# Optimization experiments

Measured on AMD Instinct MI355X. Metric: run time of the kernel, lower is better.

Reference implementation:

```python
import jax, jax.numpy as jnp
import numpy as np

N_NODES = 50000
N_EDGES = 800000
NODE_DIM = 128
EMBED_DIM = 128


def _gcn_conv(x, W, b, src, dst):
    """GCNConv: y = D^{-1/2} (A + I) D^{-1/2} X W + b (unit edge weights)."""
    n = x.shape[0]
    xw = x @ W  # [N, out]
    loop = jnp.arange(n, dtype=src.dtype)
    src2 = jnp.concatenate([src, loop])  # self-loops appended
    dst2 = jnp.concatenate([dst, loop])
    w2 = jnp.ones(src2.shape[0], dtype=xw.dtype)
    deg = jax.ops.segment_sum(w2, dst2, num_segments=n)
    dinv = jnp.where(deg > 0, jax.lax.rsqrt(deg), jnp.zeros_like(deg))
    norm = dinv[src2] * w2 * dinv[dst2]  # [E+N]
    out = jax.ops.segment_sum(norm[:, None] * xw[src2], dst2, num_segments=n)
    return out + b


def setup_inputs() -> dict:
    key = jax.random.key(0)
    ks = jax.random.split(key, 20)
    inp = {
        'node_feat': jax.random.normal(ks[0], (N_NODES, NODE_DIM), dtype=jnp.float32),
        'src': jax.random.randint(ks[1], (N_EDGES,), 0, N_NODES, dtype=jnp.int64) if jax.config.jax_enable_x64 else jax.random.randint(ks[1], (N_EDGES,), 0, N_NODES),
        'dst': jax.random.randint(ks[2], (N_EDGES,), 0, N_NODES),
        'h': jax.random.normal(ks[3], (N_NODES, EMBED_DIM), dtype=jnp.float32),
    }
    sc_in = 1.0 / np.sqrt(NODE_DIM)
    sc_2e = 1.0 / np.sqrt(2 * EMBED_DIM)
    sc_e = 1.0 / np.sqrt(EMBED_DIM)
    # conv weight/bias + gate linear weight/bias for z, r, h gates
    for i, g in enumerate(['z', 'r', 'hh']):
        inp[f'Wc_{g}'] = jax.random.normal(ks[4 + 4 * i], (NODE_DIM, EMBED_DIM), dtype=jnp.float32) * sc_in
        inp[f'bc_{g}'] = jnp.zeros((EMBED_DIM,), dtype=jnp.float32)
        inp[f'Wl_{g}'] = jax.random.normal(ks[5 + 4 * i], (2 * EMBED_DIM, EMBED_DIM), dtype=jnp.float32) * sc_2e
        inp[f'bl_{g}'] = jnp.zeros((EMBED_DIM,), dtype=jnp.float32)
    inp['W_lin'] = jax.random.normal(ks[16], (EMBED_DIM, EMBED_DIM), dtype=jnp.float32) * sc_e
    inp['b_lin'] = jnp.zeros((EMBED_DIM,), dtype=jnp.float32)
    return inp


def reference(node_feat, src, dst, h,
              Wc_z, bc_z, Wl_z, bl_z,
              Wc_r, bc_r, Wl_r, bl_r,
              Wc_hh, bc_hh, Wl_hh, bl_hh,
              W_lin, b_lin):
    # TGCN GRU cell
    cz = _gcn_conv(node_feat, Wc_z, bc_z, src, dst)
    Z = jax.nn.sigmoid(jnp.concatenate([cz, h], axis=1) @ Wl_z + bl_z)
    cr = _gcn_conv(node_feat, Wc_r, bc_r, src, dst)
    R = jax.nn.sigmoid(jnp.concatenate([cr, h], axis=1) @ Wl_r + bl_r)
    ch = _gcn_conv(node_feat, Wc_hh, bc_hh, src, dst)
    H_tilde = jnp.tanh(jnp.concatenate([ch, h * R], axis=1) @ Wl_hh + bl_hh)
    h_0 = Z * h + (1.0 - Z) * H_tilde
    # wrapper: relu + linear
    z_out = jax.nn.relu(h_0) @ W_lin + b_lin
    return (z_out, h_0)
```

## Files before the change

### kernel.cpp

```cpp
#include <hip/hip_runtime.h>
#include <math.h>

#define NN 50000
#define DD 128
#define EE 800000

typedef __attribute__((ext_vector_type(8))) short short8;
typedef __attribute__((ext_vector_type(4))) float f32x4;

__device__ __forceinline__ ushort f2bf(float f) {
    union { float f; unsigned u; } v; v.f = f;
    unsigned r = v.u + 0x7FFF + ((v.u >> 16) & 1);
    return (ushort)(r >> 16);
}

__global__ void k_cvt_deg(const float* __restrict__ X, ushort* __restrict__ Xb,
                          const int* __restrict__ dste, int* __restrict__ deg) {
    int i = blockIdx.x * 256 + threadIdx.x;
    float4 v = ((const float4*)X)[i];
    ushort4 u;
    u.x = f2bf(v.x); u.y = f2bf(v.y); u.z = f2bf(v.z); u.w = f2bf(v.w);
    ((ushort4*)Xb)[i] = u;
    if (i < EE) atomicAdd(&deg[dste[i]], 1);
}

__global__ void k_alloc(const int* __restrict__ deg, int* __restrict__ off,
                        int* __restrict__ cursor, float* __restrict__ dinv) {
    int n = blockIdx.x * 256 + threadIdx.x;
    int lane = threadIdx.x & 63;
    int d = (n < NN) ? deg[n] : 0;
    int x = d;
    #pragma unroll
    for (int o = 1; o < 64; o <<= 1) {
        int y = __shfl_up(x, o);
        if (lane >= o) x += y;
    }
    int total = __shfl(x, 63);
    int base = 0;
    if (lane == 0) base = atomicAdd(cursor, total);
    base = __shfl(base, 0);
    if (n < NN) {
        off[n] = base + x - d;
        dinv[n] = rsqrtf((float)d + 1.0f);
    }
}

__global__ void k_fill(const int* __restrict__ src, const int* __restrict__ dst,
                       const int* __restrict__ off, int* __restrict__ cur,
                       int* __restrict__ csr) {
    int e = blockIdx.x * 256 + threadIdx.x;
    if (e < EE) {
        int d = dst[e];
        int slot = atomicAdd(&cur[d], 1);
        csr[off[d] + slot] = src[e];
    }
}

__global__ __launch_bounds__(256) void k_gather(const ushort* __restrict__ Xb,
                                                const int* __restrict__ csr,
                                                const int* __restrict__ off,
                                                const int* __restrict__ deg,
                                                const float* __restrict__ dinv,
                                                ushort* __restrict__ AXb) {
    int tid = blockIdx.x * 256 + threadIdx.x;
    int n = tid >> 6, lane = tid & 63;
    if (n >= NN) return;
    float dd = dinv[n];
    uint a = *((const uint*)(Xb + (size_t)n * 128 + lane * 2));
    float acc0 = dd * dd * __uint_as_float(a << 16);
    float acc1 = dd * dd * __uint_as_float(a & 0xffff0000u);
    int o = off[n], cnt = deg[n];
    int i = 0;
    for (; i + 8 <= cnt; i += 8) {
        int s[8];
        #pragma unroll
        for (int u = 0; u < 8; u++) s[u] = csr[o + i + u];
        uint v[8];
        #pragma unroll
        for (int u = 0; u < 8; u++) v[u] = *((const uint*)(Xb + (size_t)s[u] * 128 + lane * 2));
        float c[8];
        #pragma unroll
        for (int u = 0; u < 8; u++) c[u] = dinv[s[u]] * dd;
        #pragma unroll
        for (int u = 0; u < 8; u++) {
            acc0 += c[u] * __uint_as_float(v[u] << 16);
            acc1 += c[u] * __uint_as_float(v[u] & 0xffff0000u);
        }
    }
    for (; i < cnt; i++) {
        int s = csr[o + i];
        float c = dinv[s] * dd;
        uint v = *((const uint*)(Xb + (size_t)s * 128 + lane * 2));
        acc0 += c * __uint_as_float(v << 16);
        acc1 += c * __uint_as_float(v & 0xffff0000u);
    }
    ushort2 u2; u2.x = f2bf(acc0); u2.y = f2bf(acc1);
    *((ushort2*)(AXb + (size_t)n * 128 + lane * 2)) = u2;
}

__global__ void k_prep(const float* __restrict__ Wc_z, const float* __restrict__ Wl_z,
                       const float* __restrict__ bc_z, const float* __restrict__ bl_z,
                       const float* __restrict__ Wc_r, const float* __restrict__ Wl_r,
                       const float* __restrict__ bc_r, const float* __restrict__ bl_r,
                       const float* __restrict__ Wc_h, const float* __restrict__ Wl_h,
                       const float* __restrict__ bc_h, const float* __restrict__ bl_h,
                       const float* __restrict__ W_lin,
                       ushort* __restrict__ WAs, ushort* __restrict__ WBs,
                       ushort* __restrict__ WLs, float* __restrict__ bA,
                       float* __restrict__ bB) {
    int idx = blockIdx.x * 256 + threadIdx.x;
    if (idx < 65536) {
        int k = idx >> 8, c = idx & 255, cc = c & 127;
        const float* Wc = (c < 128) ? Wc_z : Wc_r;
        const float* Wl = (c < 128) ? Wl_z : Wl_r;
        float v;
        if (k < 128) {
            float s = 0.f;
            for (int j = 0; j < 128; j++) s += Wc[k * 128 + j] * Wl[j * 128 + cc];
            v = s;
        } else {
            v = Wl[k * 128 + cc];
        }
        WAs[(k >> 5) * 8192 + (c >> 4) * 512 + (((k >> 3) & 3) * 16 + (c & 15)) * 8 + (k & 7)] = f2bf(v);
    } else if (idx < 98304) {
        int i2 = idx - 65536;
        int k = i2 >> 7, c = i2 & 127;
        float v;
        if (k < 128) {
            float s = 0.f;
            for (int j = 0; j < 128; j++) s += Wc_h[k * 128 + j] * Wl_h[j * 128 + c];
            v = s;
        } else {
            v = Wl_h[k * 128 + c];
        }
        WBs[(k >> 5) * 4096 + (c >> 4) * 512 + (((k >> 3) & 3) * 16 + (c & 15)) * 8 + (k & 7)] = f2bf(v);
    } else if (idx < 114688) {
        int i3 = idx - 98304;
        int k = i3 >> 7, c = i3 & 127;
        WLs[(k >> 5) * 4096 + (c >> 4) * 512 + (((k >> 3) & 3) * 16 + (c & 15)) * 8 + (k & 7)] = f2bf(W_lin[k * 128 + c]);
    } else if (idx < 114944) {
        int c = idx - 114688, cc = c & 127;
        const float* bc = (c < 128) ? bc_z : bc_r;
        const float* Wl = (c < 128) ? Wl_z : Wl_r;
        const float* bl = (c < 128) ? bl_z : bl_r;
        float s = bl[cc];
        for (int j = 0; j < 128; j++) s += bc[j] * Wl[j * 128 + cc];
        bA[c] = s;
    } else if (idx < 115072) {
        int c = idx - 114944;
        float s = bl_h[c];
        for (int j = 0; j < 128; j++) s += bc_h[j] * Wl_h[j * 128 + c];
        bB[c] = s;
    }
}

__global__ __launch_bounds__(256) void k_fused(const ushort* __restrict__ AXb,
                                               const float* __restrict__ h,
                                               const ushort* __restrict__ WAs,
                                               const ushort* __restrict__ WBs,
                                               const ushort* __restrict__ WLs,
                                               const float* __restrict__ bA,
                                               const float* __restrict__ bB,
                                               const float* __restrict__ b_lin,
                                               float* __restrict__ out_z,
                                               float* __restrict__ out_h) {
    __shared__ uint4 WbufV[2][1024];
    __shared__ __align__(16) ushort hRbuf[8192];

    const int tid = threadIdx.x;
    const int row0 = blockIdx.x * 64;
    const int lane = tid & 63, w = tid >> 6;
    const int tx = lane & 15, g = lane >> 4;
    const int arow = w * 16 + tx;
    const int gar = row0 + arow;
    const int drow = w * 16 + g * 4;
    const int aswz = (arow & 7) << 4;

    short8 z8 = {0, 0, 0, 0, 0, 0, 0, 0};
    short8 axf[4], hf[4];
    bool av = (gar < NN);
    #pragma unroll
    for (int ks = 0; ks < 4; ks++)
        axf[ks] = av ? *((const short8*)(AXb + (size_t)gar * 128 + ks * 32 + g * 8)) : z8;
    {
        const float4* hp = (const float4*)(h + (size_t)gar * 128);
        #pragma unroll
        for (int ks = 0; ks < 4; ks++) {
            if (av) {
                float4 u0 = hp[ks * 8 + g * 2];
                float4 u1 = hp[ks * 8 + g * 2 + 1];
                short8 t;
                t[0] = (short)f2bf(u0.x); t[1] = (short)f2bf(u0.y);
                t[2] = (short)f2bf(u0.z); t[3] = (short)f2bf(u0.w);
                t[4] = (short)f2bf(u1.x); t[5] = (short)f2bf(u1.y);
                t[6] = (short)f2bf(u1.z); t[7] = (short)f2bf(u1.w);
                hf[ks] = t;
            } else hf[ks] = z8;
        }
    }

    uint4 sr[4];
    const uint4* gwA = (const uint4*)WAs;

    #pragma unroll
    for (int j = 0; j < 4; j++) sr[j] = gwA[j * 256 + tid];
    #pragma unroll
    for (int j = 0; j < 4; j++) WbufV[0][j * 256 + tid] = sr[j];
    #pragma unroll
    for (int j = 0; j < 4; j++) sr[j] = gwA[1024 + j * 256 + tid];
    __syncthreads();

    f32x4 accA[16];
    #pragma unroll
    for (int ct = 0; ct < 16; ct++) accA[ct] = (f32x4){0.f, 0.f, 0.f, 0.f};

    #pragma unroll
    for (int ks = 0; ks < 8; ks++) {
        const int cur = ks & 1, nxt = cur ^ 1;
        if (ks < 7) {
            #pragma unroll
            for (int j = 0; j < 4; j++) WbufV[nxt][j * 256 + tid] = sr[j];
        }
        if (ks < 6) {
            #pragma unroll
            for (int j = 0; j < 4; j++) sr[j] = gwA[(ks + 2) * 1024 + j * 256 + tid];
        }
        const ushort* wbp = (const ushort*)WbufV[cur];
        short8 a = (ks < 4) ? axf[ks] : hf[ks - 4];
        #pragma unroll
        for (int ct = 0; ct < 16; ct++) {
            short8 b = *((const short8*)(wbp + ct * 512 + lane * 8));
            accA[ct] = __builtin_amdgcn_mfma_f32_16x16x32_bf16(a, b, accA[ct], 0, 0, 0);
        }
        __syncthreads();
    }

    float Zv[8][4], hv[8][4];
    #pragma unroll
    for (int ct = 0; ct < 8; ct++) {
        float bias = bA[ct * 16 + tx];
        #pragma unroll
        for (int r = 0; r < 4; r++)
            Zv[ct][r] = 1.f / (1.f + expf(-(accA[ct][r] + bias)));
    }
    #pragma unroll
    for (int ct = 0; ct < 8; ct++) {
        int cc = ct * 16 + tx;
        float bias = bA[128 + cc];
        #pragma unroll
        for (int r = 0; r < 4; r++) {
            int rr = drow + r, gr = row0 + rr;
            float hval = (gr < NN) ? h[(size_t)gr * 128 + cc] : 0.f;
            hv[ct][r] = hval;
            float R = 1.f / (1.f + expf(-(accA[8 + ct][r] + bias)));
            *((ushort*)((char*)hRbuf + rr * 256 + ((cc * 2) ^ ((rr & 7) << 4)))) = f2bf(hval * R);
        }
    }

    const uint4* gwB = (const uint4*)WBs;
    #pragma unroll
    for (int j = 0; j < 2; j++) sr[j] = gwB[j * 256 + tid];
    #pragma unroll
    for (int j = 0; j < 2; j++) WbufV[0][j * 256 + tid] = sr[j];
    #pragma unroll
    for (int j = 0; j < 2; j++) sr[j] = gwB[512 + j * 256 + tid];
    __syncthreads();

    f32x4 accB[8];
    #pragma unroll
    for (int ct = 0; ct < 8; ct++) accB[ct] = (f32x4){0.f, 0.f, 0.f, 0.f};

    #pragma unroll
    for (int ks = 0; ks < 8; ks++) {
        const int cur = ks & 1, nxt = cur ^ 1;
        if (ks < 7) {
            #pragma unroll
            for (int j = 0; j < 2; j++) WbufV[nxt][j * 256 + tid] = sr[j];
        }
        if (ks < 6) {
            #pragma unroll
            for (int j = 0; j < 2; j++) sr[j] = gwB[(ks + 2) * 512 + j * 256 + tid];
        }
        const ushort* wbp = (const ushort*)WbufV[cur];
        short8 a;
        if (ks < 4) {
            a = axf[ks];
        } else {
            int kk = ks - 4;
            a = *((const short8*)((const char*)hRbuf + arow * 256 + ((kk * 64 + g * 16) ^ aswz)));
        }
        #pragma unroll
        for (int ct = 0; ct < 8; ct++) {
            short8 b = *((const short8*)(wbp + ct * 512 + lane * 8));
            accB[ct] = __builtin_amdgcn_mfma_f32_16x16x32_bf16(a, b, accB[ct], 0, 0, 0);
        }
        __syncthreads();
    }

    #pragma unroll
    for (int ct = 0; ct < 8; ct++) {
        int cc = ct * 16 + tx;
        float bias = bB[cc];
        #pragma unroll
        for (int r = 0; r < 4; r++) {
            int rr = drow + r, gr = row0 + rr;
            float gv = accB[ct][r] + bias;
            float H = tanhf(gv);
            float Z = Zv[ct][r];
            float h0 = Z * hv[ct][r] + (1.f - Z) * H;
            if (gr < NN) out_h[(size_t)gr * 128 + cc] = h0;
            *((ushort*)((char*)hRbuf + rr * 256 + ((cc * 2) ^ ((rr & 7) << 4)))) = f2bf(fmaxf(h0, 0.f));
        }
    }

    const uint4* gwL = (const uint4*)WLs;
    #pragma unroll
    for (int j = 0; j < 2; j++) sr[j] = gwL[j * 256 + tid];
    #pragma unroll
    for (int j = 0; j < 2; j++) WbufV[0][j * 256 + tid] = sr[j];
    #pragma unroll
    for (int j = 0; j < 2; j++) sr[j] = gwL[512 + j * 256 + tid];
    __syncthreads();

    f32x4 accC[8];
    #pragma unroll
    for (int ct = 0; ct < 8; ct++) accC[ct] = (f32x4){0.f, 0.f, 0.f, 0.f};

    #pragma unroll
    for (int ks = 0; ks < 4; ks++) {
        const int cur = ks & 1, nxt = cur ^ 1;
        if (ks < 3) {
            #pragma unroll
            for (int j = 0; j < 2; j++) WbufV[nxt][j * 256 + tid] = sr[j];
        }
        if (ks < 2) {
            #pragma unroll
            for (int j = 0; j < 2; j++) sr[j] = gwL[(ks + 2) * 512 + j * 256 + tid];
        }
        const ushort* wbp = (const ushort*)WbufV[cur];
        short8 a = *((const short8*)((const char*)hRbuf + arow * 256 + ((ks * 64 + g * 16) ^ aswz)));
        #pragma unroll
        for (int ct = 0; ct < 8; ct++) {
            short8 b = *((const short8*)(wbp + ct * 512 + lane * 8));
            accC[ct] = __builtin_amdgcn_mfma_f32_16x16x32_bf16(a, b, accC[ct], 0, 0, 0);
        }
        __syncthreads();
    }

    #pragma unroll
    for (int ct = 0; ct < 8; ct++) {
        int cc = ct * 16 + tx;
        float bias = b_lin[cc];
        #pragma unroll
        for (int r = 0; r < 4; r++) {
            int gr = row0 + drow + r;
            if (gr < NN) out_z[(size_t)gr * 128 + cc] = accC[ct][r] + bias;
        }
    }
}


extern "C" void kernel_launch(void* const* d_in, const int* in_sizes, int n_in,
                              void* d_out, int out_size, void* d_ws, size_t ws_size,
                              hipStream_t stream) {
    const float* X    = (const float*)d_in[0];
    const int*   src  = (const int*)d_in[1];
    const int*   dst  = (const int*)d_in[2];
    const float* h    = (const float*)d_in[3];
    const float* Wc_z = (const float*)d_in[4];
    const float* bc_z = (const float*)d_in[5];
    const float* Wl_z = (const float*)d_in[6];
    const float* bl_z = (const float*)d_in[7];
    const float* Wc_r = (const float*)d_in[8];
    const float* bc_r = (const float*)d_in[9];
    const float* Wl_r = (const float*)d_in[10];
    const float* bl_r = (const float*)d_in[11];
    const float* Wc_h = (const float*)d_in[12];
    const float* bc_h = (const float*)d_in[13];
    const float* Wl_h = (const float*)d_in[14];
    const float* bl_h = (const float*)d_in[15];
    const float* W_lin = (const float*)d_in[16];
    const float* b_lin = (const float*)d_in[17];

    float* out_z = (float*)d_out;
    float* out_h = out_z + (size_t)NN * DD;

    float* ws = (float*)d_ws;
    float*  dinv   = ws;
    int*    deg    = (int*)(ws + 50048);
    int*    cur    = (int*)(ws + 100096);
    int*    cursor = (int*)(ws + 150144);
    int*    off    = (int*)(ws + 150208);
    int*    csr    = (int*)(ws + 200256);
    float*  bA     = ws + 1000320;
    float*  bB     = ws + 1000576;
    ushort* WAs    = (ushort*)(ws + 1000704);
    ushort* WBs    = (ushort*)(ws + 1033472);
    ushort* WLs    = (ushort*)(ws + 1049856);
    ushort* AXb    = (ushort*)(ws + 1058048);
    ushort* Xb     = (ushort*)(ws + 4258048);

    hipMemsetAsync(deg, 0, 100160 * sizeof(int), stream);
    k_prep<<<450, 256, 0, stream>>>(Wc_z, Wl_z, bc_z, bl_z, Wc_r, Wl_r, bc_r, bl_r,
                                    Wc_h, Wl_h, bc_h, bl_h, W_lin,
                                    WAs, WBs, WLs, bA, bB);
    k_cvt_deg<<<6250, 256, 0, stream>>>(X, Xb, dst, deg);
    k_alloc<<<196, 256, 0, stream>>>(deg, off, cursor, dinv);
    k_fill<<<3125, 256, 0, stream>>>(src, dst, off, cur, csr);
    k_gather<<<12500, 256, 0, stream>>>(Xb, csr, off, deg, dinv, AXb);
    k_fused<<<782, 256, 0, stream>>>(AXb, h, WAs, WBs, WLs, bA, bB, b_lin, out_z, out_h);
}
```

Baseline: 350.8 us.

## Split fused GRU GEMM into three persistent kernels with register-resident weights

Replaces the single fused per-64-row GEMM kernel with three persistent kernels (gates Z/R, candidate H, output linear). Each keeps its weight fragments in registers and grid-strides over 16-row subtiles, so weights are no longer streamed through LDS for every block. Also merges the X/h bf16 conversion with weight prep into one launch, and has the CSR fill use a precomputed cursor instead of off+slot. The cost is extra global traffic for the Zt, hR and relu intermediates and two more kernel launches.

```diff
diff --git a/kernel.cpp b/kernel.cpp
--- a/kernel.cpp
+++ b/kernel.cpp
@@ -4,6 +4,7 @@
 #define NN 50000
 #define DD 128
 #define EE 800000
+#define NSUB 3125
 
 typedef __attribute__((ext_vector_type(8))) short short8;
 typedef __attribute__((ext_vector_type(4))) float f32x4;
@@ -13,102 +14,42 @@
     unsigned r = v.u + 0x7FFF + ((v.u >> 16) & 1);
     return (ushort)(r >> 16);
 }
-
-__global__ void k_cvt_deg(const float* __restrict__ X, ushort* __restrict__ Xb,
-                          const int* __restrict__ dste, int* __restrict__ deg) {
-    int i = blockIdx.x * 256 + threadIdx.x;
-    float4 v = ((const float4*)X)[i];
-    ushort4 u;
-    u.x = f2bf(v.x); u.y = f2bf(v.y); u.z = f2bf(v.z); u.w = f2bf(v.w);
-    ((ushort4*)Xb)[i] = u;
-    if (i < EE) atomicAdd(&deg[dste[i]], 1);
-}
-
-__global__ void k_alloc(const int* __restrict__ deg, int* __restrict__ off,
-                        int* __restrict__ cursor, float* __restrict__ dinv) {
-    int n = blockIdx.x * 256 + threadIdx.x;
-    int lane = threadIdx.x & 63;
-    int d = (n < NN) ? deg[n] : 0;
-    int x = d;
-    #pragma unroll
-    for (int o = 1; o < 64; o <<= 1) {
-        int y = __shfl_up(x, o);
-        if (lane >= o) x += y;
-    }
-    int total = __shfl(x, 63);
-    int base = 0;
-    if (lane == 0) base = atomicAdd(cursor, total);
-    base = __shfl(base, 0);
-    if (n < NN) {
-        off[n] = base + x - d;
-        dinv[n] = rsqrtf((float)d + 1.0f);
-    }
-}
-
-__global__ void k_fill(const int* __restrict__ src, const int* __restrict__ dst,
-                       const int* __restrict__ off, int* __restrict__ cur,
-                       int* __restrict__ csr) {
-    int e = blockIdx.x * 256 + threadIdx.x;
-    if (e < EE) {
-        int d = dst[e];
-        int slot = atomicAdd(&cur[d], 1);
-        csr[off[d] + slot] = src[e];
-    }
-}
-
-__global__ __launch_bounds__(256) void k_gather(const ushort* __restrict__ Xb,
-                                                const int* __restrict__ csr,
-                                                const int* __restrict__ off,
-                                                const int* __restrict__ deg,
-                                                const float* __restrict__ dinv,
-                                                ushort* __restrict__ AXb) {
-    int tid = blockIdx.x * 256 + threadIdx.x;
-    int n = tid >> 6, lane = tid & 63;
-    if (n >= NN) return;
-    float dd = dinv[n];
-    uint a = *((const uint*)(Xb + (size_t)n * 128 + lane * 2));
-    float acc0 = dd * dd * __uint_as_float(a << 16);
-    float acc1 = dd * dd * __uint_as_float(a & 0xffff0000u);
-    int o = off[n], cnt = deg[n];
-    int i = 0;
-    for (; i + 8 <= cnt; i += 8) {
-        int s[8];
-        #pragma unroll
-        for (int u = 0; u < 8; u++) s[u] = csr[o + i + u];
-        uint v[8];
-        #pragma unroll
-        for (int u = 0; u < 8; u++) v[u] = *((const uint*)(Xb + (size_t)s[u] * 128 + lane * 2));
-        float c[8];
-        #pragma unroll
-        for (int u = 0; u < 8; u++) c[u] = dinv[s[u]] * dd;
-        #pragma unroll
-        for (int u = 0; u < 8; u++) {
-            acc0 += c[u] * __uint_as_float(v[u] << 16);
-            acc1 += c[u] * __uint_as_float(v[u] & 0xffff0000u);
-        }
-    }
-    for (; i < cnt; i++) {
-        int s = csr[o + i];
-        float c = dinv[s] * dd;
-        uint v = *((const uint*)(Xb + (size_t)s * 128 + lane * 2));
-        acc0 += c * __uint_as_float(v << 16);
-        acc1 += c * __uint_as_float(v & 0xffff0000u);
-    }
-    ushort2 u2; u2.x = f2bf(acc0); u2.y = f2bf(acc1);
-    *((ushort2*)(AXb + (size_t)n * 128 + lane * 2)) = u2;
-}
-
-__global__ void k_prep(const float* __restrict__ Wc_z, const float* __restrict__ Wl_z,
-                       const float* __restrict__ bc_z, const float* __restrict__ bl_z,
-                       const float* __restrict__ Wc_r, const float* __restrict__ Wl_r,
-                       const float* __restrict__ bc_r, const float* __restrict__ bl_r,
-                       const float* __restrict__ Wc_h, const float* __restrict__ Wl_h,
-                       const float* __restrict__ bc_h, const float* __restrict__ bl_h,
-                       const float* __restrict__ W_lin,
-                       ushort* __restrict__ WAs, ushort* __restrict__ WBs,
-                       ushort* __restrict__ WLs, float* __restrict__ bA,
-                       float* __restrict__ bB) {
-    int idx = blockIdx.x * 256 + threadIdx.x;
+__device__ __forceinline__ float bf2f(ushort u) {
+    return __uint_as_float(((unsigned)u) << 16);
+}
+__device__ __forceinline__ float sigm(float x) { return 1.f / (1.f + expf(-x)); }
+
+__global__ void k_cvtprep(const float* __restrict__ X, ushort* __restrict__ Xb,
+                          const float* __restrict__ h, ushort* __restrict__ hb,
+                          const int* __restrict__ dste, int* __restrict__ deg,
+                          const float* __restrict__ Wc_z, const float* __restrict__ Wl_z,
+                          const float* __restrict__ bc_z, const float* __restrict__ bl_z,
+                          const float* __restrict__ Wc_r, const float* __restrict__ Wl_r,
+                          const float* __restrict__ bc_r, const float* __restrict__ bl_r,
+                          const float* __restrict__ Wc_h, const float* __restrict__ Wl_h,
+                          const float* __restrict__ bc_h, const float* __restrict__ bl_h,
+                          const float* __restrict__ W_lin,
+                          ushort* __restrict__ WAs, ushort* __restrict__ WBs,
+                          ushort* __restrict__ WLs, float* __restrict__ bA,
+                          float* __restrict__ bB) {
+    if (blockIdx.x < 6250) {
+        int i = blockIdx.x * 256 + threadIdx.x;
+        float4 v = ((const float4*)X)[i];
+        ushort4 u;
+        u.x = f2bf(v.x); u.y = f2bf(v.y); u.z = f2bf(v.z); u.w = f2bf(v.w);
+        ((ushort4*)Xb)[i] = u;
+        if (i < EE) atomicAdd(&deg[dste[i]], 1);
+        return;
+    }
+    if (blockIdx.x < 12500) {
+        int i = (blockIdx.x - 6250) * 256 + threadIdx.x;
+        float4 v = ((const float4*)h)[i];
+        ushort4 u;
+        u.x = f2bf(v.x); u.y = f2bf(v.y); u.z = f2bf(v.z); u.w = f2bf(v.w);
+        ((ushort4*)hb)[i] = u;
+        return;
+    }
+    int idx = (blockIdx.x - 12500) * 256 + threadIdx.x;
     if (idx < 65536) {
         int k = idx >> 8, c = idx & 255, cc = c & 127;
         const float* Wc = (c < 128) ? Wc_z : Wc_r;
@@ -154,207 +95,270 @@
     }
 }
 
-__global__ __launch_bounds__(256) void k_fused(const ushort* __restrict__ AXb,
-                                               const float* __restrict__ h,
-                                               const ushort* __restrict__ WAs,
-                                               const ushort* __restrict__ WBs,
-                                               const ushort* __restrict__ WLs,
-                                               const float* __restrict__ bA,
-                                               const float* __restrict__ bB,
-                                               const float* __restrict__ b_lin,
-                                               float* __restrict__ out_z,
-                                               float* __restrict__ out_h) {
-    __shared__ uint4 WbufV[2][1024];
-    __shared__ __align__(16) ushort hRbuf[8192];
-
-    const int tid = threadIdx.x;
-    const int row0 = blockIdx.x * 64;
-    const int lane = tid & 63, w = tid >> 6;
+__global__ void k_alloc(const int* __restrict__ deg, int* __restrict__ off,
+                        int* __restrict__ cur, int* __restrict__ cursor,
+                        float* __restrict__ dinv) {
+    int n = blockIdx.x * 256 + threadIdx.x;
+    int lane = threadIdx.x & 63;
+    int d = (n < NN) ? deg[n] : 0;
+    int x = d;
+    #pragma unroll
+    for (int o = 1; o < 64; o <<= 1) {
+        int y = __shfl_up(x, o);
+        if (lane >= o) x += y;
+    }
+    int total = __shfl(x, 63);
+    int base = 0;
+    if (lane == 0) base = atomicAdd(cursor, total);
+    base = __shfl(base, 0);
+    if (n < NN) {
+        int o2 = base + x - d;
+        off[n] = o2;
+        cur[n] = o2;
+        dinv[n] = rsqrtf((float)d + 1.0f);
+    }
+}
+
+__global__ void k_fill(const int* __restrict__ src, const int* __restrict__ dst,
+                       int* __restrict__ cur, int* __restrict__ csr) {
+    int e = blockIdx.x * 256 + threadIdx.x;
+    if (e < EE) {
+        int slot = atomicAdd(&cur[dst[e]], 1);
+        csr[slot] = src[e];
+    }
+}
+
+__global__ __launch_bounds__(256) void k_gather(const ushort* __restrict__ Xb,
+                                                const int* __restrict__ csr,
+                                                const int* __restrict__ off,
+                                                const int* __restrict__ deg,
+                                                const float* __restrict__ dinv,
+                                                ushort* __restrict__ AXb) {
+    int tid = blockIdx.x * 256 + threadIdx.x;
+    int n = tid >> 6, lane = tid & 63;
+    if (n >= NN) return;
+    int o   = __builtin_amdgcn_readfirstlane(off[n]);
+    int cnt = __builtin_amdgcn_readfirstlane(deg[n]);
+    float dd = dinv[n];
+    uint a = *((const uint*)(Xb + (size_t)n * 128 + lane * 2));
+    float acc0 = dd * dd * __uint_as_float(a << 16);
+    float acc1 = dd * dd * __uint_as_float(a & 0xffff0000u);
+    int i = 0;
+    for (; i + 8 <= cnt; i += 8) {
+        int s[8];
+        #pragma unroll
+        for (int u = 0; u < 8; u++) s[u] = csr[o + i + u];
+        uint v[8];
+        #pragma unroll
+        for (int u = 0; u < 8; u++) v[u] = *((const uint*)(Xb + (size_t)s[u] * 128 + lane * 2));
+        float c[8];
+        #pragma unroll
+        for (int u = 0; u < 8; u++) c[u] = dinv[s[u]] * dd;
+        #pragma unroll
+        for (int u = 0; u < 8; u++) {
+            acc0 += c[u] * __uint_as_float(v[u] << 16);
+            acc1 += c[u] * __uint_as_float(v[u] & 0xffff0000u);
+        }
+    }
+    for (; i < cnt; i++) {
+        int s = csr[o + i];
+        float c = dinv[s] * dd;
+        uint v = *((const uint*)(Xb + (size_t)s * 128 + lane * 2));
+        acc0 += c * __uint_as_float(v << 16);
+        acc1 += c * __uint_as_float(v & 0xffff0000u);
+    }
+    ushort2 u2; u2.x = f2bf(acc0); u2.y = f2bf(acc1);
+    *((ushort2*)(AXb + (size_t)n * 128 + lane * 2)) = u2;
+}
+
+__global__ __launch_bounds__(256, 2) void k_gemmA(const ushort* __restrict__ AXb,
+                                                  const ushort* __restrict__ hb,
+                                                  const float* __restrict__ h,
+                                                  const ushort* __restrict__ WAs,
+                                                  const float* __restrict__ bA,
+                                                  ushort* __restrict__ Zt,
+                                                  ushort* __restrict__ hRb) {
+    __shared__ ushort scr[4][1024];
+    const int tid = threadIdx.x, lane = tid & 63, w = tid >> 6;
     const int tx = lane & 15, g = lane >> 4;
-    const int arow = w * 16 + tx;
-    const int gar = row0 + arow;
-    const int drow = w * 16 + g * 4;
-    const int aswz = (arow & 7) << 4;
-
-    short8 z8 = {0, 0, 0, 0, 0, 0, 0, 0};
-    short8 axf[4], hf[4];
-    bool av = (gar < NN);
-    #pragma unroll
-    for (int ks = 0; ks < 4; ks++)
-        axf[ks] = av ? *((const short8*)(AXb + (size_t)gar * 128 + ks * 32 + g * 8)) : z8;
-    {
-        const float4* hp = (const float4*)(h + (size_t)gar * 128);
+
+    short8 wf[4][8];
+    #pragma unroll
+    for (int ct = 0; ct < 4; ct++)
+        #pragma unroll
+        for (int ks = 0; ks < 8; ks++)
+            wf[ct][ks] = *((const short8*)(WAs + ks * 8192 + (w * 4 + ct) * 512 + lane * 8));
+    float bias[4];
+    #pragma unroll
+    for (int ct = 0; ct < 4; ct++) bias[ct] = bA[w * 64 + ct * 16 + tx];
+
+    for (int rs = blockIdx.x; rs < NSUB; rs += gridDim.x) {
+        const int arow = rs * 16 + tx;
+        short8 axf[4], hf[4];
         #pragma unroll
         for (int ks = 0; ks < 4; ks++) {
-            if (av) {
-                float4 u0 = hp[ks * 8 + g * 2];
-                float4 u1 = hp[ks * 8 + g * 2 + 1];
-                short8 t;
-                t[0] = (short)f2bf(u0.x); t[1] = (short)f2bf(u0.y);
-                t[2] = (short)f2bf(u0.z); t[3] = (short)f2bf(u0.w);
-                t[4] = (short)f2bf(u1.x); t[5] = (short)f2bf(u1.y);
-                t[6] = (short)f2bf(u1.z); t[7] = (short)f2bf(u1.w);
-                hf[ks] = t;
-            } else hf[ks] = z8;
-        }
-    }
-
-    uint4 sr[4];
-    const uint4* gwA = (const uint4*)WAs;
-
-    #pragma unroll
-    for (int j = 0; j < 4; j++) sr[j] = gwA[j * 256 + tid];
-    #pragma unroll
-    for (int j = 0; j < 4; j++) WbufV[0][j * 256 + tid] = sr[j];
-    #pragma unroll
-    for (int j = 0; j < 4; j++) sr[j] = gwA[1024 + j * 256 + tid];
-    __syncthreads();
-
-    f32x4 accA[16];
-    #pragma unroll
-    for (int ct = 0; ct < 16; ct++) accA[ct] = (f32x4){0.f, 0.f, 0.f, 0.f};
-
-    #pragma unroll
-    for (int ks = 0; ks < 8; ks++) {
-        const int cur = ks & 1, nxt = cur ^ 1;
-        if (ks < 7) {
-            #pragma unroll
-            for (int j = 0; j < 4; j++) WbufV[nxt][j * 256 + tid] = sr[j];
-        }
-        if (ks < 6) {
-            #pragma unroll
-            for (int j = 0; j < 4; j++) sr[j] = gwA[(ks + 2) * 1024 + j * 256 + tid];
-        }
-        const ushort* wbp = (const ushort*)WbufV[cur];
-        short8 a = (ks < 4) ? axf[ks] : hf[ks - 4];
-        #pragma unroll
-        for (int ct = 0; ct < 16; ct++) {
-            short8 b = *((const short8*)(wbp + ct * 512 + lane * 8));
-            accA[ct] = __builtin_amdgcn_mfma_f32_16x16x32_bf16(a, b, accA[ct], 0, 0, 0);
-        }
-        __syncthreads();
-    }
-
-    float Zv[8][4], hv[8][4];
-    #pragma unroll
-    for (int ct = 0; ct < 8; ct++) {
-        float bias = bA[ct * 16 + tx];
-        #pragma unroll
-        for (int r = 0; r < 4; r++)
-            Zv[ct][r] = 1.f / (1.f + expf(-(accA[ct][r] + bias)));
-    }
-    #pragma unroll
-    for (int ct = 0; ct < 8; ct++) {
-        int cc = ct * 16 + tx;
-        float bias = bA[128 + cc];
-        #pragma unroll
-        for (int r = 0; r < 4; r++) {
-            int rr = drow + r, gr = row0 + rr;
-            float hval = (gr < NN) ? h[(size_t)gr * 128 + cc] : 0.f;
-            hv[ct][r] = hval;
-            float R = 1.f / (1.f + expf(-(accA[8 + ct][r] + bias)));
-            *((ushort*)((char*)hRbuf + rr * 256 + ((cc * 2) ^ ((rr & 7) << 4)))) = f2bf(hval * R);
-        }
-    }
-
-    const uint4* gwB = (const uint4*)WBs;
-    #pragma unroll
-    for (int j = 0; j < 2; j++) sr[j] = gwB[j * 256 + tid];
-    #pragma unroll
-    for (int j = 0; j < 2; j++) WbufV[0][j * 256 + tid] = sr[j];
-    #pragma unroll
-    for (int j = 0; j < 2; j++) sr[j] = gwB[512 + j * 256 + tid];
-    __syncthreads();
-
-    f32x4 accB[8];
-    #pragma unroll
-    for (int ct = 0; ct < 8; ct++) accB[ct] = (f32x4){0.f, 0.f, 0.f, 0.f};
-
-    #pragma unroll
-    for (int ks = 0; ks < 8; ks++) {
-        const int cur = ks & 1, nxt = cur ^ 1;
-        if (ks < 7) {
-            #pragma unroll
-            for (int j = 0; j < 2; j++) WbufV[nxt][j * 256 + tid] = sr[j];
-        }
-        if (ks < 6) {
-            #pragma unroll
-            for (int j = 0; j < 2; j++) sr[j] = gwB[(ks + 2) * 512 + j * 256 + tid];
-        }
-        const ushort* wbp = (const ushort*)WbufV[cur];
-        short8 a;
-        if (ks < 4) {
-            a = axf[ks];
+            axf[ks] = *((const short8*)(AXb + (size_t)arow * 128 + ks * 32 + g * 8));
+            hf[ks]  = *((const short8*)(hb  + (size_t)arow * 128 + ks * 32 + g * 8));
+        }
+        f32x4 acc[4];
+        #pragma unroll
+        for (int ct = 0; ct < 4; ct++) acc[ct] = (f32x4){0.f, 0.f, 0.f, 0.f};
+        #pragma unroll
+        for (int ks = 0; ks < 4; ks++)
+            #pragma unroll
+            for (int ct = 0; ct < 4; ct++)
+                acc[ct] = __builtin_amdgcn_mfma_f32_16x16x32_bf16(axf[ks], wf[ct][ks], acc[ct], 0, 0, 0);
+        #pragma unroll
+        for (int ks = 0; ks < 4; ks++)
+            #pragma unroll
+            for (int ct = 0; ct < 4; ct++)
+                acc[ct] = __builtin_amdgcn_mfma_f32_16x16x32_bf16(hf[ks], wf[ct][4 + ks], acc[ct], 0, 0, 0);
+
+        const int r0 = rs * 16 + g * 4;
+        if (w < 2) {
+            #pragma unroll
+            for (int ct = 0; ct < 4; ct++) {
+                int col = w * 64 + ct * 16 + tx;
+                ushort4 z4;
+                z4.x = f2bf(sigm(acc[ct][0] + bias[ct]));
+                z4.y = f2bf(sigm(acc[ct][1] + bias[ct]));
+                z4.z = f2bf(sigm(acc[ct][2] + bias[ct]));
+                z4.w = f2bf(sigm(acc[ct][3] + bias[ct]));
+                *((ushort4*)(Zt + (size_t)col * NN + r0)) = z4;
+            }
         } else {
-            int kk = ks - 4;
-            a = *((const short8*)((const char*)hRbuf + arow * 256 + ((kk * 64 + g * 16) ^ aswz)));
-        }
-        #pragma unroll
-        for (int ct = 0; ct < 8; ct++) {
-            short8 b = *((const short8*)(wbp + ct * 512 + lane * 8));
-            accB[ct] = __builtin_amdgcn_mfma_f32_16x16x32_bf16(a, b, accB[ct], 0, 0, 0);
-        }
-        __syncthreads();
-    }
-
-    #pragma unroll
-    for (int ct = 0; ct < 8; ct++) {
-        int cc = ct * 16 + tx;
-        float bias = bB[cc];
-        #pragma unroll
-        for (int r = 0; r < 4; r++) {
-            int rr = drow + r, gr = row0 + rr;
-            float gv = accB[ct][r] + bias;
-            float H = tanhf(gv);
-            float Z = Zv[ct][r];
-            float h0 = Z * hv[ct][r] + (1.f - Z) * H;
-            if (gr < NN) out_h[(size_t)gr * 128 + cc] = h0;
-            *((ushort*)((char*)hRbuf + rr * 256 + ((cc * 2) ^ ((rr & 7) << 4)))) = f2bf(fmaxf(h0, 0.f));
-        }
-    }
-
-    const uint4* gwL = (const uint4*)WLs;
-    #pragma unroll
-    for (int j = 0; j < 2; j++) sr[j] = gwL[j * 256 + tid];
-    #pragma unroll
-    for (int j = 0; j < 2; j++) WbufV[0][j * 256 + tid] = sr[j];
-    #pragma unroll
-    for (int j = 0; j < 2; j++) sr[j] = gwL[512 + j * 256 + tid];
-    __syncthreads();
-
-    f32x4 accC[8];
-    #pragma unroll
-    for (int ct = 0; ct < 8; ct++) accC[ct] = (f32x4){0.f, 0.f, 0.f, 0.f};
-
-    #pragma unroll
-    for (int ks = 0; ks < 4; ks++) {
-        const int cur = ks & 1, nxt = cur ^ 1;
-        if (ks < 3) {
-            #pragma unroll
-            for (int j = 0; j < 2; j++) WbufV[nxt][j * 256 + tid] = sr[j];
-        }
-        if (ks < 2) {
-            #pragma unroll
-            for (int j = 0; j < 2; j++) sr[j] = gwL[(ks + 2) * 512 + j * 256 + tid];
-        }
-        const ushort* wbp = (const ushort*)WbufV[cur];
-        short8 a = *((const short8*)((const char*)hRbuf + arow * 256 + ((ks * 64 + g * 16) ^ aswz)));
-        #pragma unroll
-        for (int ct = 0; ct < 8; ct++) {
-            short8 b = *((const short8*)(wbp + ct * 512 + lane * 8));
-            accC[ct] = __builtin_amdgcn_mfma_f32_16x16x32_bf16(a, b, accC[ct], 0, 0, 0);
-        }
-        __syncthreads();
-    }
-
-    #pragma unroll
-    for (int ct = 0; ct < 8; ct++) {
-        int cc = ct * 16 + tx;
-        float bias = b_lin[cc];
-        #pragma unroll
-        for (int r = 0; r < 4; r++) {
-            int gr = row0 + drow + r;
-            if (gr < NN) out_z[(size_t)gr * 128 + cc] = accC[ct][r] + bias;
+            #pragma unroll
+            for (int ct = 0; ct < 4; ct++) {
+                int cl = ct * 16 + tx;
+                int cc = (w - 2) * 64 + cl;
+                #pragma unroll
+                for (int r = 0; r < 4; r++) {
+                    float hval = h[(size_t)(r0 + r) * 128 + cc];
+                    float R = sigm(acc[ct][r] + bias[ct]);
+                    scr[w][(g * 4 + r) * 64 + cl] = f2bf(hval * R);
+                }
+            }
+            int c0 = lane, c1 = lane + 64;
+            short8 t0 = *((const short8*)(&scr[w][(c0 >> 3) * 64 + (c0 & 7) * 8]));
+            short8 t1 = *((const short8*)(&scr[w][(c1 >> 3) * 64 + (c1 & 7) * 8]));
+            *((short8*)(hRb + (size_t)(rs * 16 + (c0 >> 3)) * 128 + (w - 2) * 64 + (c0 & 7) * 8)) = t0;
+            *((short8*)(hRb + (size_t)(rs * 16 + (c1 >> 3)) * 128 + (w - 2) * 64 + (c1 & 7) * 8)) = t1;
+        }
+    }
+}
+
+__global__ __launch_bounds__(256, 2) void k_gemmB(const ushort* __restrict__ AXb,
+                                                  const ushort* __restrict__ hRb,
+                                                  const float* __restrict__ h,
+                                                  const ushort* __restrict__ Zt,
+                                                  const ushort* __restrict__ WBs,
+                                                  const float* __restrict__ bB,
+                                                  float* __restrict__ out_h,
+                                                  ushort* __restrict__ rl) {
+    __shared__ float scrf[4][512];
+    const int tid = threadIdx.x, lane = tid & 63, w = tid >> 6;
+    const int tx = lane & 15, g = lane >> 4;
+
+    short8 wf[2][8];
+    #pragma unroll
+    for (int ct = 0; ct < 2; ct++)
+        #pragma unroll
+        for (int ks = 0; ks < 8; ks++)
+            wf[ct][ks] = *((const short8*)(WBs + ks * 4096 + (w * 2 + ct) * 512 + lane * 8));
+    float bias[2];
+    #pragma unroll
+    for (int ct = 0; ct < 2; ct++) bias[ct] = bB[w * 32 + ct * 16 + tx];
+
+    for (int rs = blockIdx.x; rs < NSUB; rs += gridDim.x) {
+        const int arow = rs * 16 + tx;
+        short8 axf[4], hrf[4];
+        #pragma unroll
+        for (int ks = 0; ks < 4; ks++) {
+            axf[ks] = *((const short8*)(AXb + (size_t)arow * 128 + ks * 32 + g * 8));
+            hrf[ks] = *((const short8*)(hRb + (size_t)arow * 128 + ks * 32 + g * 8));
+        }
+        f32x4 acc[2];
+        #pragma unroll
+        for (int ct = 0; ct < 2; ct++) acc[ct] = (f32x4){0.f, 0.f, 0.f, 0.f};
+        #pragma unroll
+        for (int ks = 0; ks < 4; ks++)
+            #pragma unroll
+            for (int ct = 0; ct < 2; ct++)
+                acc[ct] = __builtin_amdgcn_mfma_f32_16x16x32_bf16(axf[ks], wf[ct][ks], acc[ct], 0, 0, 0);
+        #pragma unroll
+        for (int ks = 0; ks < 4; ks++)
+            #pragma unroll
+            for (int ct = 0; ct < 2; ct++)
+                acc[ct] = __builtin_amdgcn_mfma_f32_16x16x32_bf16(hrf[ks], wf[ct][4 + ks], acc[ct], 0, 0, 0);
+
+        const int r0 = rs * 16 + g * 4;
+        #pragma unroll
+        for (int ct = 0; ct < 2; ct++) {
+            int col = w * 32 + ct * 16 + tx;
+            ushort4 z4 = *((const ushort4*)(Zt + (size_t)col * NN + r0));
+            float zz[4] = {bf2f(z4.x), bf2f(z4.y), bf2f(z4.z), bf2f(z4.w)};
+            #pragma unroll
+            for (int r = 0; r < 4; r++) {
+                float hval = h[(size_t)(r0 + r) * 128 + col];
+                float H = tanhf(acc[ct][r] + bias[ct]);
+                float h0 = zz[r] * hval + (1.f - zz[r]) * H;
+                scrf[w][(g * 4 + r) * 32 + ct * 16 + tx] = h0;
+            }
+        }
+        int row = lane >> 2, cb = (lane & 3) * 8;
+        float4 h0a = *((const float4*)(&scrf[w][row * 32 + cb]));
+        float4 h0b = *((const float4*)(&scrf[w][row * 32 + cb + 4]));
+        size_t go = (size_t)(rs * 16 + row) * 128 + w * 32 + cb;
+        *((float4*)(out_h + go)) = h0a;
+        *((float4*)(out_h + go + 4)) = h0b;
+        short8 rv;
+        rv[0] = (short)f2bf(fmaxf(h0a.x, 0.f)); rv[1] = (short)f2bf(fmaxf(h0a.y, 0.f));
+        rv[2] = (short)f2bf(fmaxf(h0a.z, 0.f)); rv[3] = (short)f2bf(fmaxf(h0a.w, 0.f));
+        rv[4] = (short)f2bf(fmaxf(h0b.x, 0.f)); rv[5] = (short)f2bf(fmaxf(h0b.y, 0.f));
+        rv[6] = (short)f2bf(fmaxf(h0b.z, 0.f)); rv[7] = (short)f2bf(fmaxf(h0b.w, 0.f));
+        *((short8*)(rl + go)) = rv;
+    }
+}
+
+__global__ __launch_bounds__(256, 4) void k_gemmC(const ushort* __restrict__ rl,
+                                                  const ushort* __restrict__ WLs,
+                                                  const float* __restrict__ b_lin,
+                                                  float* __restrict__ out_z) {
+    const int tid = threadIdx.x, lane = tid & 63, w = tid >> 6;
+    const int tx = lane & 15, g = lane >> 4;
+
+    short8 wf[2][4];
+    #pragma unroll
+    for (int ct = 0; ct < 2; ct++)
+        #pragma unroll
+        for (int ks = 0; ks < 4; ks++)
+            wf[ct][ks] = *((const short8*)(WLs + ks * 4096 + (w * 2 + ct) * 512 + lane * 8));
+    float bias[2];
+    #pragma unroll
+    for (int ct = 0; ct < 2; ct++) bias[ct] = b_lin[w * 32 + ct * 16 + tx];
+
+    for (int rs = blockIdx.x; rs < NSUB; rs += gridDim.x) {
+        const int arow = rs * 16 + tx;
+        short8 rlf[4];
+        #pragma unroll
+        for (int ks = 0; ks < 4; ks++)
+            rlf[ks] = *((const short8*)(rl + (size_t)arow * 128 + ks * 32 + g * 8));
+        f32x4 acc[2];
+        #pragma unroll
+        for (int ct = 0; ct < 2; ct++) acc[ct] = (f32x4){0.f, 0.f, 0.f, 0.f};
+        #pragma unroll
+        for (int ks = 0; ks < 4; ks++)
+            #pragma unroll
+            for (int ct = 0; ct < 2; ct++)
+                acc[ct] = __builtin_amdgcn_mfma_f32_16x16x32_bf16(rlf[ks], wf[ct][ks], acc[ct], 0, 0, 0);
+
+        const int r0 = rs * 16 + g * 4;
+        #pragma unroll
+        for (int ct = 0; ct < 2; ct++) {
+            int col = w * 32 + ct * 16 + tx;
+            #pragma unroll
+            for (int r = 0; r < 4; r++)
+                out_z[(size_t)(r0 + r) * 128 + col] = acc[ct][r] + bias[ct];
         }
     }
 }
@@ -399,14 +403,20 @@
     ushort* WLs    = (ushort*)(ws + 1049856);
     ushort* AXb    = (ushort*)(ws + 1058048);
     ushort* Xb     = (ushort*)(ws + 4258048);
+    ushort* Zt     = Xb;
+    ushort* hb     = (ushort*)(ws + 7458048);
+    ushort* rl     = hb;
+    ushort* hRb    = (ushort*)(ws + 10658048);
 
     hipMemsetAsync(deg, 0, 100160 * sizeof(int), stream);
-    k_prep<<<450, 256, 0, stream>>>(Wc_z, Wl_z, bc_z, bl_z, Wc_r, Wl_r, bc_r, bl_r,
-                                    Wc_h, Wl_h, bc_h, bl_h, W_lin,
-                                    WAs, WBs, WLs, bA, bB);
-    k_cvt_deg<<<6250, 256, 0, stream>>>(X, Xb, dst, deg);
-    k_alloc<<<196, 256, 0, stream>>>(deg, off, cursor, dinv);
-    k_fill<<<3125, 256, 0, stream>>>(src, dst, off, cur, csr);
+    k_cvtprep<<<12950, 256, 0, stream>>>(X, Xb, h, hb, dst, deg,
+                                         Wc_z, Wl_z, bc_z, bl_z, Wc_r, Wl_r, bc_r, bl_r,
+                                         Wc_h, Wl_h, bc_h, bl_h, W_lin,
+                                         WAs, WBs, WLs, bA, bB);
+    k_alloc<<<196, 256, 0, stream>>>(deg, off, cur, cursor, dinv);
+    k_fill<<<3125, 256, 0, stream>>>(src, dst, cur, csr);
     k_gather<<<12500, 256, 0, stream>>>(Xb, csr, off, deg, dinv, AXb);
-    k_fused<<<782, 256, 0, stream>>>(AXb, h, WAs, WBs, WLs, bA, bB, b_lin, out_z, out_h);
-}
+    k_gemmA<<<512, 256, 0, stream>>>(AXb, hb, h, WAs, bA, Zt, hRb);
+    k_gemmB<<<512, 256, 0, stream>>>(AXb, hRb, h, Zt, WBs, bB, out_h, rl);
+    k_gemmC<<<1024, 256, 0, stream>>>(rl, WLs, b_lin, out_z);
+}
```

Result: faster. 327.3 us (-6.7%).
